# Performance work log

Hardware: AMD Instinct MI355X
Metric: run time of the kernel (lower is better)

The kernel has to match this reference:

```python
import jax, jax.numpy as jnp
import numpy as np

N = 8192
C = 128
K = 20          # neighbors per dilation branch
DILS = (1, 2)   # dilations
K_FULL = K * max(DILS)  # neighbors in the base knn graph
R = 4           # upsampling ratio
N_IDGCN = 2     # inception blocks
NEG_SLOPE_CONV = 0.2
NEG_SLOPE_MLP = 0.01  # torch LeakyReLU default in reconstructor


def knn_idx(pos, k):
    # brute-force knn on [N,3]; exclude self by taking k+1 and dropping col 0
    sq = jnp.sum(pos * pos, axis=-1)                       # [N]
    d = sq[:, None] + sq[None, :] - 2.0 * (pos @ pos.T)    # [N,N]
    _, idx = jax.lax.top_k(-d, k + 1)                      # nearest first
    return idx[:, 1:]                                      # [N,k]


def edge_conv(x, idx, W, b):
    # EdgeConv: max_j LeakyReLU(W @ [x_i, x_j - x_i] + b)
    xj = x[idx]                                            # [N,k,C] gather
    xi = jnp.broadcast_to(x[:, None, :], xj.shape)
    e = jnp.concatenate([xi, xj - xi], axis=-1)            # [N,k,2C]
    h = jax.nn.leaky_relu(e @ W + b, NEG_SLOPE_CONV)
    return jnp.max(h, axis=1)                              # [N,Cout]


def setup_inputs() -> dict:
    key = jax.random.key(0)
    ks = jax.random.split(key, 10)
    s_lift = 1.0 / np.sqrt(6.0)
    s_gcn = 1.0 / np.sqrt(2.0 * C)
    s_mlp = 1.0 / np.sqrt(C)
    n_gcn = N_IDGCN * len(DILS)
    return {
        "x": jax.random.normal(ks[0], (N, 3), dtype=jnp.float32),
        "W0": jax.random.normal(ks[1], (6, C), dtype=jnp.float32) * s_lift,
        "b0": jnp.zeros((C,), dtype=jnp.float32),
        "Wg": jax.random.normal(ks[2], (n_gcn, 2 * C, C), dtype=jnp.float32) * s_gcn,
        "bg": jnp.zeros((n_gcn, C), dtype=jnp.float32),
        "Wu": jax.random.normal(ks[3], (2 * C, R * C), dtype=jnp.float32) * s_gcn,
        "bu": jnp.zeros((R * C,), dtype=jnp.float32),
        "Wr1": jax.random.normal(ks[4], (C, C), dtype=jnp.float32) * s_mlp,
        "br1": jnp.zeros((C,), dtype=jnp.float32),
        "Wr2": jax.random.normal(ks[5], (C, 3), dtype=jnp.float32) * s_mlp,
        "br2": jnp.zeros((3,), dtype=jnp.float32),
    }


def reference(x, W0, b0, Wg, bg, Wu, bu, Wr1, br1, Wr2, br2):
    pos = x
    # knn graph on positions (k * max(dilations) neighbors)
    idx = knn_idx(pos, K_FULL)                             # [N, K_FULL]
    # lift 3 -> C with an EdgeConv on the first K neighbors
    h = edge_conv(pos, idx[:, :K], W0, b0)                 # [N, C]
    # Inception DenseGCN feature extractor: dilated EdgeConv branches + residual
    li = 0
    for _ in range(N_IDGCN):
        acc = jnp.zeros_like(h)
        for d in DILS:
            idx_d = idx[:, ::d][:, :K]                     # dilated neighbors
            acc = acc + edge_conv(h, idx_d, Wg[li], bg[li])
            li += 1
        h = h + acc / float(len(DILS))                     # residual
    # NodeShuffle upsampler: EdgeConv to r*C then shuffle nodes
    u = edge_conv(h, idx[:, :K], Wu, bu)                   # [N, r*C]
    u = u.reshape(N * R, C)                                # [N*r, C]
    # reconstructor MLP -> 3D coordinates
    q = jax.nn.leaky_relu(u @ Wr1 + br1, NEG_SLOPE_MLP)
    q = q @ Wr2 + br2                                      # [N*r, 3]
    return q
```

## Files before the change

kernel.cpp:

```cpp
#include <hip/hip_runtime.h>
#include <math.h>

#define N_PTS 8192
#define KFULL 40
#define KNB 20
#define QB 8
#define KBLK 512
#define NBK 1024
#define CAP 512

typedef unsigned short u16;
typedef unsigned int u32;
typedef unsigned long long u64;
typedef __attribute__((ext_vector_type(8))) short bf16x8;
typedef __attribute__((ext_vector_type(4))) float f32x4;
typedef __attribute__((ext_vector_type(2))) float f32x2;

__device__ __forceinline__ u16 f2b(float v) {
  u32 u = __float_as_uint(v);
  return (u16)((u + 0x7FFFu + ((u >> 16) & 1u)) >> 16);
}
__device__ __forceinline__ float b2f(u16 b) {
  return __uint_as_float(((u32)b) << 16);
}
__device__ __forceinline__ u32 pk2(float a, float b) {
  return (u32)f2b(a) | ((u32)f2b(b) << 16);
}
__device__ __forceinline__ u32 dmap(float d) {
  u32 b = __float_as_uint(d);
  return b ^ ((u32)(((int)b) >> 31) | 0x80000000u);
}
__device__ __forceinline__ float inv_edge(int b) {
  if (b >= 1022) return 3.4e38f;
  const u32 m = (((u32)(b + 1)) << 22) - 1u;
  if (m < 0x80000000u) return 0.f;
  return __uint_as_float(m - 0x80000000u);
}
__device__ __forceinline__ void maxu4(const uint4 v, float m[8]) {
  m[0] = fmaxf(m[0], __uint_as_float(v.x << 16));
  m[1] = fmaxf(m[1], __uint_as_float(v.x & 0xFFFF0000u));
  m[2] = fmaxf(m[2], __uint_as_float(v.y << 16));
  m[3] = fmaxf(m[3], __uint_as_float(v.y & 0xFFFF0000u));
  m[4] = fmaxf(m[4], __uint_as_float(v.z << 16));
  m[5] = fmaxf(m[5], __uint_as_float(v.z & 0xFFFF0000u));
  m[6] = fmaxf(m[6], __uint_as_float(v.w << 16));
  m[7] = fmaxf(m[7], __uint_as_float(v.w & 0xFFFF0000u));
}
__device__ __forceinline__ void unp4(const uint4 v, float p[8]) {
  p[0] = __uint_as_float(v.x << 16);
  p[1] = __uint_as_float(v.x & 0xFFFF0000u);
  p[2] = __uint_as_float(v.y << 16);
  p[3] = __uint_as_float(v.y & 0xFFFF0000u);
  p[4] = __uint_as_float(v.z << 16);
  p[5] = __uint_as_float(v.z & 0xFFFF0000u);
  p[6] = __uint_as_float(v.w << 16);
  p[7] = __uint_as_float(v.w & 0xFFFF0000u);
}

typedef const __attribute__((address_space(1))) unsigned int* gas_p;
typedef __attribute__((address_space(3))) unsigned int* las_p;
__device__ __forceinline__ void gll16(const void* g, void* l) {
  __builtin_amdgcn_global_load_lds((gas_p)g, (las_p)l, 16, 0, 0);
}

__device__ __forceinline__ f32x2 pdist(const f32x2 qx2, const f32x2 qy2,
                                       const f32x2 qz2, const f32x2 qs2,
                                       const float4 p) {
  const f32x2 px = {p.x, p.x}, py = {p.y, p.y}, pz = {p.z, p.z};
  const f32x2 pw = {p.w, p.w};
  return __builtin_elementwise_fma(
      qx2, px,
      __builtin_elementwise_fma(
          qy2, py, __builtin_elementwise_fma(qz2, pz, qs2 + pw)));
}

__device__ __forceinline__ void scan_cut(const u32 (*hist)[NBK], int* s_cut,
                                         int t) {
  const int w = t >> 6, lane = t & 63;
  if (w < QB / 2) {
    const u32* H = hist[w];
    const int base = lane * (NBK / 64);
    u32 lsum = 0;
#pragma unroll
    for (int k = 0; k < NBK / 64; ++k) lsum += H[base + k];
    u32 inc = lsum;
#pragma unroll
    for (int off = 1; off < 64; off <<= 1) {
      const u32 u = __shfl_up(inc, off);
      if (lane >= off) inc += u;
    }
    const u32 excl = inc - lsum;
    const u32 TGT = KFULL + 1;
    const u32 exlo = excl & 0xFFFFu, inlo = inc & 0xFFFFu;
    if (exlo < TGT && inlo >= TGT) {
      u32 cum = exlo;
      for (int k = 0; k < NBK / 64; ++k) {
        cum += H[base + k] & 0xFFFFu;
        if (cum >= TGT) { s_cut[2 * w] = base + k; break; }
      }
    }
    const u32 exhi = excl >> 16, inhi = inc >> 16;
    if (exhi < TGT && inhi >= TGT) {
      u32 cum = exhi;
      for (int k = 0; k < NBK / 64; ++k) {
        cum += H[base + k] >> 16;
        if (cum >= TGT) { s_cut[2 * w + 1] = base + k; break; }
      }
    }
  }
}

__device__ __forceinline__ int scan_cut_wave(const u32* H, int lane) {
  const int base = lane * (NBK / 64);
  u32 lsum = 0;
#pragma unroll
  for (int k = 0; k < NBK / 64; ++k) lsum += H[base + k];
  u32 inc = lsum;
#pragma unroll
  for (int off = 1; off < 64; off <<= 1) {
    const u32 u = __shfl_up(inc, off);
    if (lane >= off) inc += u;
  }
  const u32 excl = inc - lsum;
  int cut = -1;
  if (excl < 41u && inc >= 41u) {
    u32 cum = excl;
    for (int k = 0; k < NBK / 64; ++k) {
      cum += H[base + k];
      if (cum >= 41u) { cut = base + k; break; }
    }
  }
  const u64 mask = __ballot(cut >= 0);
  if (mask == 0ull) return NBK - 1;
  const int src = __ffsll((long long)mask) - 1;
  return __shfl(cut, src);
}

__global__ __launch_bounds__(KBLK) void knn_kernel(const float4* __restrict__ pos4,
                                                   int* __restrict__ idx_out) {
  __shared__ __align__(16) u32 hmem[2 * QB * CAP];
  u32 (*hist)[NBK] = (u32(*)[NBK])hmem;
  u64 (*cand)[CAP] = (u64(*)[CAP])hmem;
  __shared__ float4 s_q[QB];
  __shared__ int s_cut[QB];
  __shared__ int s_cnt[QB];

  const int qb = blockIdx.x * QB, t = threadIdx.x;
  if (t < QB) {
    s_q[t] = pos4[qb + t];
    s_cnt[t] = 0;
  }
  for (int b = t; b < 4 * NBK; b += KBLK) hmem[b] = 0;
  __syncthreads();

  f32x2 qx2[4], qy2[4], qz2[4], qs2[4];
#pragma unroll
  for (int qp = 0; qp < 4; ++qp) {
    const float4 v0 = s_q[2 * qp], v1 = s_q[2 * qp + 1];
    qx2[qp] = (f32x2){-2.0f * v0.x, -2.0f * v1.x};
    qy2[qp] = (f32x2){-2.0f * v0.y, -2.0f * v1.y};
    qz2[qp] = (f32x2){-2.0f * v0.z, -2.0f * v1.z};
    qs2[qp] = (f32x2){v0.w, v1.w};
  }

  {
    const int j = t << 4;
    const float4 p = pos4[j];
#pragma unroll
    for (int qp = 0; qp < 4; ++qp) {
      const f32x2 d2 = pdist(qx2[qp], qy2[qp], qz2[qp], qs2[qp], p);
      atomicAdd(&hist[qp][dmap(d2.x) >> 22], 1u);
      atomicAdd(&hist[qp][dmap(d2.y) >> 22], 0x10000u);
    }
  }
  __syncthreads();
  scan_cut(hist, s_cut, t);
  __syncthreads();
  float r2a[QB];
#pragma unroll
  for (int q = 0; q < QB; ++q) r2a[q] = inv_edge(s_cut[q]);
  for (int b = t; b < 4 * NBK; b += KBLK) hmem[b] = 0;
  __syncthreads();

#pragma unroll 2
  for (int s = 0; s < 16; ++s) {
    const int j = t + (s << 9);
    const float4 p = pos4[j];
#pragma unroll
    for (int qp = 0; qp < 4; ++qp) {
      const f32x2 d2 = pdist(qx2[qp], qy2[qp], qz2[qp], qs2[qp], p);
      if (d2.x <= r2a[2 * qp]) atomicAdd(&hist[qp][dmap(d2.x) >> 22], 1u);
      if (d2.y <= r2a[2 * qp + 1]) atomicAdd(&hist[qp][dmap(d2.y) >> 22], 0x10000u);
    }
  }
  __syncthreads();
  scan_cut(hist, s_cut, t);
  __syncthreads();
  float r2b[QB];
#pragma unroll
  for (int q = 0; q < QB; ++q) r2b[q] = inv_edge(s_cut[q]);

#pragma unroll 2
  for (int s = 0; s < 16; ++s) {
    const int j = t + (s << 9);
    const float4 p = pos4[j];
#pragma unroll
    for (int qp = 0; qp < 4; ++qp) {
      const f32x2 d2 = pdist(qx2[qp], qy2[qp], qz2[qp], qs2[qp], p);
      if (d2.x <= r2b[2 * qp]) {
        const int slot = atomicAdd(&s_cnt[2 * qp], 1);
        if (slot < CAP)
          cand[2 * qp][slot] = ((u64)dmap(d2.x) << 13) | (u64)j;
      }
      if (d2.y <= r2b[2 * qp + 1]) {
        const int slot = atomicAdd(&s_cnt[2 * qp + 1], 1);
        if (slot < CAP)
          cand[2 * qp + 1][slot] = ((u64)dmap(d2.y) << 13) | (u64)j;
      }
    }
  }
  __syncthreads();

  {
    const int w = t >> 6, lane = t & 63;
    int cnt = s_cnt[w];
    if (cnt > CAP) {
      const float4 qv = s_q[w];
      const float ax = -2.0f * qv.x, ay = -2.0f * qv.y, az = -2.0f * qv.z;
      const float aw = qv.w;
      const float R2w = inv_edge(s_cut[w]);
      u32* fbh = (u32*)cand[w];
      for (int b = lane; b < NBK; b += 64) fbh[b] = 0;
      for (int j = lane; j < N_PTS; j += 64) {
        const float4 p = pos4[j];
        const float d = fmaf(ax, p.x, fmaf(ay, p.y, fmaf(az, p.z, aw + p.w)));
        if (d <= R2w) atomicAdd(&fbh[dmap(d) >> 22], 1u);
      }
      const int cut2 = scan_cut_wave(fbh, lane);
      const float R2r = inv_edge(cut2);
      int base = 0;
      for (int j0 = 0; j0 < N_PTS; j0 += 64) {
        const int j = j0 + lane;
        const float4 p = pos4[j];
        const float d = fmaf(ax, p.x, fmaf(ay, p.y, fmaf(az, p.z, aw + p.w)));
        const bool pred = (d <= R2r);
        const u64 mask = __ballot(pred);
        if (pred) {
          const int off = __popcll(mask & ((1ull << lane) - 1ull));
          if (base + off < CAP)
            cand[w][base + off] = ((u64)dmap(d) << 13) | (u64)j;
        }
        base += (int)__popcll(mask);
      }
      cnt = base;
    }
    const int cmax = cnt < CAP ? cnt : CAP;
    if (cmax <= 192) {
      const u64 FK = ~0ull;
      const u64 my0 = (lane < cmax) ? cand[w][lane] : FK;
      const u64 my1 = (lane + 64 < cmax) ? cand[w][lane + 64] : FK;
      const u64 my2 = (lane + 128 < cmax) ? cand[w][lane + 128] : FK;
      int rk0 = 0, rk1 = 0, rk2 = 0;
      for (int c = 0; c < cmax; ++c) {
        const u64 bc = cand[w][c];
        rk0 += (bc < my0) ? 1 : 0;
        rk1 += (bc < my1) ? 1 : 0;
        rk2 += (bc < my2) ? 1 : 0;
      }
      if (lane < cmax && rk0 >= 1 && rk0 <= KFULL)
        idx_out[(qb + w) * KFULL + (rk0 - 1)] = (int)(my0 & 0x1FFFull);
      if (lane + 64 < cmax && rk1 >= 1 && rk1 <= KFULL)
        idx_out[(qb + w) * KFULL + (rk1 - 1)] = (int)(my1 & 0x1FFFull);
      if (lane + 128 < cmax && rk2 >= 1 && rk2 <= KFULL)
        idx_out[(qb + w) * KFULL + (rk2 - 1)] = (int)(my2 & 0x1FFFull);
    } else {
      for (int c0 = lane; c0 < cmax; c0 += 64) {
        const u64 my = cand[w][c0];
        int rank = 0;
        for (int c = 0; c < cmax; ++c) rank += (cand[w][c] < my) ? 1 : 0;
        if (rank >= 1 && rank <= KFULL)
          idx_out[(qb + w) * KFULL + (rank - 1)] = (int)(my & 0x1FFFull);
      }
    }
  }
}

__device__ __forceinline__ void wcvt_body(const float* __restrict__ src,
                                          u16* __restrict__ dst, int ncols,
                                          int rows_per_tensor, int elems_per_tensor,
                                          int rg, int k) {
  const int li = rg / rows_per_tensor;
  const int r = rg % rows_per_tensor;
  const float* s = src + (size_t)li * elems_per_tensor;
  u16* d = dst + (size_t)li * elems_per_tensor;
  const int part = r / ncols, col = r % ncols;
  d[(size_t)r * 128 + k] = f2b(s[(size_t)(part * 128 + k) * ncols + col]);
}

__global__ __launch_bounds__(128) void prep_kernel(
    const float* __restrict__ x, const float* __restrict__ W0,
    const float* __restrict__ b0, const float* __restrict__ Wg,
    const float* __restrict__ Wu, const float* __restrict__ Wr1,
    float* __restrict__ Aout, u16* __restrict__ Pout, u16* __restrict__ Wgb,
    u16* __restrict__ Wub, u16* __restrict__ Wr1b, float4* __restrict__ pos4) {
  const int b = blockIdx.x, t = threadIdx.x;
  if (b < 8192) {
    const float px = x[b * 3 + 0], py = x[b * 3 + 1], pz = x[b * 3 + 2];
    const float a = b0[t] + px * W0[t] + py * W0[128 + t] + pz * W0[256 + t];
    const float p = px * W0[384 + t] + py * W0[512 + t] + pz * W0[640 + t];
    Aout[(size_t)b * 128 + t] = a;
    Pout[(size_t)b * 128 + t] = f2b(p);
  } else if (b < 9216) {
    wcvt_body(Wg, Wgb, 128, 256, 256 * 128, b - 8192, t);
  } else if (b < 10240) {
    wcvt_body(Wu, Wub, 512, 1024, 1024 * 128, b - 9216, t);
  } else if (b < 10368) {
    wcvt_body(Wr1, Wr1b, 128, 128, 128 * 128, b - 10240, t);
  } else {
    const int j = (b - 10368) * 128 + t;
    const float px = x[j * 3 + 0], py = x[j * 3 + 1], pz = x[j * 3 + 2];
    pos4[j] = make_float4(px, py, pz, px * px + py * py + pz * pz);
  }
}

__global__ __launch_bounds__(256) void gemm_mfma_kernel(
    const u16* __restrict__ Ain, const u16* __restrict__ Wt,
    const float* __restrict__ bias, int GA, int span_shift, int nAtot, int nPtot,
    float slope, int use_act, float* __restrict__ Aout,
    u16* __restrict__ Aout16, u16* __restrict__ Pout) {
  __shared__ __align__(16) u16 Al[128 * 128];
  __shared__ __align__(16) u16 Bl[64 * 128];
  const int bm = blockIdx.x * 128;
  const int bn = blockIdx.y * 64;
  const int tid = threadIdx.x;

#pragma unroll
  for (int it = 0; it < 8; ++it) {
    const int g = it * 256 + tid;
    const int row = g >> 4, cc = g & 15;
    const int sc = cc ^ (row & 7);
    gll16(Ain + (size_t)(bm + row) * 128 + sc * 8, &Al[g * 8]);
  }
#pragma unroll
  for (int it = 0; it < 4; ++it) {
    const int g = it * 256 + tid;
    const int row = g >> 4, cc = g & 15;
    const int sc = cc ^ (row & 7);
    gll16(Wt + (size_t)(bn + row) * 128 + sc * 8, &Bl[g * 8]);
  }
  __syncthreads();

  const int wv = tid >> 6, lane = tid & 63;
  const int wm = wv & 1, wn = wv >> 1;
  const int lr = lane & 15, lk = lane >> 4;

  bf16x8 a[4][4], b[2][4];
  f32x4 acc[4][2];
#pragma unroll
  for (int m = 0; m < 4; ++m)
#pragma unroll
    for (int n = 0; n < 2; ++n) acc[m][n] = (f32x4){0.f, 0.f, 0.f, 0.f};

#pragma unroll
  for (int m = 0; m < 4; ++m) {
    const int row = wm * 64 + m * 16 + lr;
#pragma unroll
    for (int ks = 0; ks < 4; ++ks) {
      const int c = ks * 4 + lk;
      a[m][ks] = *(const bf16x8*)&Al[row * 128 + (c ^ (row & 7)) * 8];
    }
  }
#pragma unroll
  for (int n = 0; n < 2; ++n) {
    const int col = wn * 32 + n * 16 + lr;
#pragma unroll
    for (int ks = 0; ks < 4; ++ks) {
      const int c = ks * 4 + lk;
      b[n][ks] = *(const bf16x8*)&Bl[col * 128 + (c ^ (col & 7)) * 8];
    }
  }

#pragma unroll
  for (int ks = 0; ks < 4; ++ks)
#pragma unroll
    for (int m = 0; m < 4; ++m)
#pragma unroll
      for (int n = 0; n < 2; ++n)
        acc[m][n] = __builtin_amdgcn_mfma_f32_16x16x32_bf16(a[m][ks], b[n][ks],
                                                            acc[m][n], 0, 0, 0);

  const int span = 1 << span_shift;
  const int GP = span - GA;
#pragma unroll
  for (int n = 0; n < 2; ++n) {
    const int col = bn + wn * 32 + n * 16 + lr;
    const int g = col >> span_shift;
    const int wi = col & (span - 1);
    const bool isA = wi < GA;
    const float bv = isA ? bias[g * GA + wi] : 0.f;
#pragma unroll
    for (int m = 0; m < 4; ++m) {
      const int row0 = bm + wm * 64 + m * 16 + lk * 4;
#pragma unroll
      for (int r = 0; r < 4; ++r) {
        float v = acc[m][n][r] + bv;
        if (isA) {
          if (use_act) v = v > 0.f ? v : v * slope;
          if (Aout16)
            Aout16[(size_t)(row0 + r) * nAtot + g * GA + wi] = f2b(v);
          else
            Aout[(size_t)(row0 + r) * nAtot + g * GA + wi] = v;
        } else {
          Pout[(size_t)(row0 + r) * nPtot + g * GP + (wi - GA)] = f2b(v);
        }
      }
    }
  }
}

__global__ __launch_bounds__(256) void gather_one_kernel(
    const float* __restrict__ A, const u16* __restrict__ P,
    const int* __restrict__ idx, int C, int dil, float* __restrict__ outf,
    u16* __restrict__ outb) {
  const int t = threadIdx.x;
  const int i = blockIdx.x * 16 + (t >> 4);
  const int c = blockIdx.y * 128 + (t & 15) * 8;
  float m[8];
#pragma unroll
  for (int k = 0; k < 8; ++k) m[k] = -INFINITY;
  const int ib = i * KFULL;
#pragma unroll
  for (int j = 0; j < KNB; ++j) {
    const int n = idx[ib + j * dil] & (N_PTS - 1);
    maxu4(*(const uint4*)&P[(size_t)n * C + c], m);
  }
  float pv[8];
  unp4(*(const uint4*)&P[(size_t)i * C + c], pv);
  const float4 a0 = *(const float4*)&A[(size_t)i * C + c];
  const float4 a1 = *(const float4*)&A[(size_t)i * C + c + 4];
  const float av[8] = {a0.x, a0.y, a0.z, a0.w, a1.x, a1.y, a1.z, a1.w};
  float v[8];
#pragma unroll
  for (int k = 0; k < 8; ++k) {
    const float x = av[k] - pv[k] + m[k];
    v[k] = x > 0.f ? x : 0.2f * x;
  }
  if (outf) {
    *(float4*)&outf[(size_t)i * C + c] = make_float4(v[0], v[1], v[2], v[3]);
    *(float4*)&outf[(size_t)i * C + c + 4] = make_float4(v[4], v[5], v[6], v[7]);
  }
  if (outb) {
    uint4 pb = {pk2(v[0], v[1]), pk2(v[2], v[3]), pk2(v[4], v[5]), pk2(v[6], v[7])};
    *(uint4*)&outb[(size_t)i * C + c] = pb;
  }
}

__global__ __launch_bounds__(256) void gather_pair_kernel(
    const float* __restrict__ Ap, const u16* __restrict__ Pp,
    const int* __restrict__ idx, float* __restrict__ h, u16* __restrict__ hb) {
  const int t = threadIdx.x;
  const int i = blockIdx.x * 16 + (t >> 4);
  const int c = (t & 15) * 8;
  float m1[8], m2[8];
#pragma unroll
  for (int k = 0; k < 8; ++k) { m1[k] = -INFINITY; m2[k] = -INFINITY; }
  const int ib = i * KFULL;
#pragma unroll
  for (int j = 0; j < KNB; ++j) {
    const int n1 = idx[ib + j] & (N_PTS - 1);
    maxu4(*(const uint4*)&Pp[(size_t)n1 * 256 + c], m1);
    const int n2 = idx[ib + 2 * j] & (N_PTS - 1);
    maxu4(*(const uint4*)&Pp[(size_t)n2 * 256 + 128 + c], m2);
  }
  float p0[8], p1[8];
  unp4(*(const uint4*)&Pp[(size_t)i * 256 + c], p0);
  unp4(*(const uint4*)&Pp[(size_t)i * 256 + 128 + c], p1);
  const float4 a00 = *(const float4*)&Ap[(size_t)i * 256 + c];
  const float4 a01 = *(const float4*)&Ap[(size_t)i * 256 + c + 4];
  const float4 a10 = *(const float4*)&Ap[(size_t)i * 256 + 128 + c];
  const float4 a11 = *(const float4*)&Ap[(size_t)i * 256 + 128 + c + 4];
  const float av0[8] = {a00.x, a00.y, a00.z, a00.w, a01.x, a01.y, a01.z, a01.w};
  const float av1[8] = {a10.x, a10.y, a10.z, a10.w, a11.x, a11.y, a11.z, a11.w};
  const float4 h0 = *(const float4*)&h[(size_t)i * 128 + c];
  const float4 h1 = *(const float4*)&h[(size_t)i * 128 + c + 4];
  const float hv[8] = {h0.x, h0.y, h0.z, h0.w, h1.x, h1.y, h1.z, h1.w};
  float v[8];
#pragma unroll
  for (int k = 0; k < 8; ++k) {
    float x1 = av0[k] - p0[k] + m1[k];
    x1 = x1 > 0.f ? x1 : 0.2f * x1;
    float x2 = av1[k] - p1[k] + m2[k];
    x2 = x2 > 0.f ? x2 : 0.2f * x2;
    v[k] = hv[k] + 0.5f * (x1 + x2);
  }
  *(float4*)&h[(size_t)i * 128 + c] = make_float4(v[0], v[1], v[2], v[3]);
  *(float4*)&h[(size_t)i * 128 + c + 4] = make_float4(v[4], v[5], v[6], v[7]);
  uint4 pb = {pk2(v[0], v[1]), pk2(v[2], v[3]), pk2(v[4], v[5]), pk2(v[6], v[7])};
  *(uint4*)&hb[(size_t)i * 128 + c] = pb;
}

__global__ __launch_bounds__(256) void recon_fused_kernel(
    const u16* __restrict__ Ab16, const u16* __restrict__ Pb16,
    const int* __restrict__ idx, const u16* __restrict__ Wr1b,
    const float* __restrict__ br1, const float* __restrict__ Wr2,
    const float* __restrict__ br2, float* __restrict__ out) {
  __shared__ __align__(16) u16 Al[128 * 128];
  __shared__ __align__(16) u16 Bl[128 * 128];
  __shared__ __align__(16) u16 Tt[128 * 132];
  __shared__ float w2s[387];
  const int b = blockIdx.x, tid = threadIdx.x;
  const int pbase = b * 32;

#pragma unroll
  for (int it = 0; it < 8; ++it) {
    const int g = it * 256 + tid;
    const int row = g >> 4, cc = g & 15;
    const int sc = cc ^ (row & 7);
    gll16(Wr1b + (size_t)row * 128 + sc * 8, &Bl[g * 8]);
  }
  if (tid < 128) {
    w2s[tid] = Wr2[tid];
    w2s[tid + 128] = Wr2[tid + 128];
    w2s[tid + 256] = Wr2[tid + 256];
  }
  if (tid < 3) w2s[384 + tid] = br2[tid];

#pragma unroll
  for (int it = 0; it < 4; ++it) {
    const int tau = it * 256 + tid;
    const int rr = tau >> 3;
    const int cg = tau & 7;
    const int pl = rr >> 2, s = rr & 3;
    const int p = pbase + pl;
    const int colb = s * 128 + cg * 16;
    float m[8], m2[8];
#pragma unroll
    for (int k = 0; k < 8; ++k) { m[k] = -INFINITY; m2[k] = -INFINITY; }
    const int ib = p * KFULL;
#pragma unroll
    for (int j = 0; j < KNB; ++j) {
      const int n = idx[ib + j] & (N_PTS - 1);
      maxu4(*(const uint4*)&Pb16[(size_t)n * 512 + colb], m);
      maxu4(*(const uint4*)&Pb16[(size_t)n * 512 + colb + 8], m2);
    }
    float av[8], av2[8], pv[8], pv2[8];
    unp4(*(const uint4*)&Ab16[(size_t)p * 512 + colb], av);
    unp4(*(const uint4*)&Ab16[(size_t)p * 512 + colb + 8], av2);
    unp4(*(const uint4*)&Pb16[(size_t)p * 512 + colb], pv);
    unp4(*(const uint4*)&Pb16[(size_t)p * 512 + colb + 8], pv2);
    float v[8], v2[8];
#pragma unroll
    for (int k = 0; k < 8; ++k) {
      float x = av[k] - pv[k] + m[k];
      v[k] = x > 0.f ? x : 0.2f * x;
      float y = av2[k] - pv2[k] + m2[k];
      v2[k] = y > 0.f ? y : 0.2f * y;
    }
    uint4 w0 = {pk2(v[0], v[1]), pk2(v[2], v[3]), pk2(v[4], v[5]), pk2(v[6], v[7])};
    uint4 w1 = {pk2(v2[0], v2[1]), pk2(v2[2], v2[3]), pk2(v2[4], v2[5]),
                pk2(v2[6], v2[7])};
    const int c0 = cg * 2, c1 = cg * 2 + 1;
    *(uint4*)&Al[rr * 128 + (c0 ^ (rr & 7)) * 8] = w0;
    *(uint4*)&Al[rr * 128 + (c1 ^ (rr & 7)) * 8] = w1;
  }
  __syncthreads();

  const int wv = tid >> 6, lane = tid & 63;
  const int wm = wv & 1, wn = wv >> 1;
  const int lr = lane & 15, lk = lane >> 4;
  f32x4 acc[4][4];
#pragma unroll
  for (int m = 0; m < 4; ++m)
#pragma unroll
    for (int n = 0; n < 4; ++n) acc[m][n] = (f32x4){0.f, 0.f, 0.f, 0.f};

#pragma unroll
  for (int ks = 0; ks < 4; ++ks) {
    const int c = ks * 4 + lk;
    bf16x8 a[4], bb[4];
#pragma unroll
    for (int m = 0; m < 4; ++m) {
      const int row = wm * 64 + m * 16 + lr;
      a[m] = *(const bf16x8*)&Al[row * 128 + (c ^ (row & 7)) * 8];
    }
#pragma unroll
    for (int n = 0; n < 4; ++n) {
      const int col = wn * 64 + n * 16 + lr;
      bb[n] = *(const bf16x8*)&Bl[col * 128 + (c ^ (col & 7)) * 8];
    }
#pragma unroll
    for (int m = 0; m < 4; ++m)
#pragma unroll
      for (int n = 0; n < 4; ++n)
        acc[m][n] = __builtin_amdgcn_mfma_f32_16x16x32_bf16(a[m], bb[n],
                                                            acc[m][n], 0, 0, 0);
  }

#pragma unroll
  for (int n = 0; n < 4; ++n) {
    const int col = wn * 64 + n * 16 + lr;
    const float bv = br1[col];
#pragma unroll
    for (int m = 0; m < 4; ++m) {
      const int row0 = wm * 64 + m * 16 + lk * 4;
#pragma unroll
      for (int r = 0; r < 4; ++r) {
        float v = acc[m][n][r] + bv;
        v = v > 0.f ? v : 0.01f * v;
        Tt[(row0 + r) * 132 + col] = f2b(v);
      }
    }
  }
  __syncthreads();

  if (tid < 128) {
    float q0 = w2s[384], q1 = w2s[385], q2 = w2s[386];
#pragma unroll 4
    for (int k = 0; k < 128; ++k) {
      const float tv = b2f(Tt[tid * 132 + k]);
      q0 = fmaf(tv, w2s[k * 3 + 0], q0);
      q1 = fmaf(tv, w2s[k * 3 + 1], q1);
      q2 = fmaf(tv, w2s[k * 3 + 2], q2);
    }
    const size_t R = (size_t)b * 128 + tid;
    out[R * 3 + 0] = q0;
    out[R * 3 + 1] = q1;
    out[R * 3 + 2] = q2;
  }
}

extern "C" void kernel_launch(void* const* d_in, const int* in_sizes, int n_in,
                              void* d_out, int out_size, void* d_ws, size_t ws_size,
                              hipStream_t stream) {
  const float* x = (const float*)d_in[0];
  const float* W0 = (const float*)d_in[1];
  const float* b0 = (const float*)d_in[2];
  const float* Wg = (const float*)d_in[3];
  const float* bg = (const float*)d_in[4];
  const float* Wu = (const float*)d_in[5];
  const float* bu = (const float*)d_in[6];
  const float* Wr1 = (const float*)d_in[7];
  const float* br1 = (const float*)d_in[8];
  const float* Wr2 = (const float*)d_in[9];
  const float* br2 = (const float*)d_in[10];
  float* out = (float*)d_out;

  char* w = (char*)d_ws;
  int* idx = (int*)(w + 0);
  float4* pos4 = (float4*)(w + 1310720);
  float* h = (float*)(w + 1441792);
  u16* hb = (u16*)(w + 5636096);
  float* Apair = (float*)(w + 7733248);
  u16* Ppair = (u16*)(w + 16121856);
  u16* Wgb = (u16*)(w + 20316160);
  u16* Wub = (u16*)(w + 20578304);
  u16* Wr1b = (u16*)(w + 20840448);
  float* Abig = (float*)(w + 20873216);
  u16* Ab16 = (u16*)(w + 20873216);
  u16* Pbig = (u16*)(w + 37650432);

  prep_kernel<<<10432, 128, 0, stream>>>(x, W0, b0, Wg, Wu, Wr1, Abig, Pbig, Wgb,
                                         Wub, Wr1b, pos4);

  knn_kernel<<<N_PTS / QB, KBLK, 0, stream>>>(pos4, idx);

  gather_one_kernel<<<dim3(512, 1), 256, 0, stream>>>(Abig, Pbig, idx, 128, 1, h, hb);

  for (int blk = 0; blk < 2; ++blk) {
    const int li = blk * 2;
    gemm_mfma_kernel<<<dim3(64, 8), 256, 0, stream>>>(
        hb, Wgb + (size_t)li * 256 * 128, bg + li * 128, 128, 8, 256, 256, 0.f, 0,
        Apair, (u16*)nullptr, Ppair);
    gather_pair_kernel<<<512, 256, 0, stream>>>(Apair, Ppair, idx, h, hb);
  }

  gemm_mfma_kernel<<<dim3(64, 16), 256, 0, stream>>>(hb, Wub, bu, 512, 10, 512, 512,
                                                     0.f, 0, (float*)nullptr, Ab16,
                                                     Pbig);

  recon_fused_kernel<<<256, 256, 0, stream>>>(Ab16, Pbig, idx, Wr1b, br1, Wr2, br2,
                                              out);
}
```

Before: 162.3 us.

## Replace two-pass histogram radius search in kNN with sampled per-lane top-4 bound

The kNN kernel no longer builds two shared-memory histograms, each with a scan, to find a distance cutoff. Each wave instead takes a 2048-point sample (every fourth point), keeps a per-lane top-4 of distance keys, and binary-searches with ballots for the 41st smallest key. That value is an upper bound on the true 41st-nearest distance and becomes the radius for a single candidate-collection pass. This removes one full distance pass and the histogram atomics, but the looser radius admits more candidates. The rank-sort fast path is widened to 256 candidates to absorb that, and the overflow fallback remains for the case of more than 512.

```diff
diff --git a/kernel.cpp b/kernel.cpp
--- a/kernel.cpp
+++ b/kernel.cpp
@@ -29,6 +29,10 @@
 __device__ __forceinline__ u32 dmap(float d) {
   u32 b = __float_as_uint(d);
   return b ^ ((u32)(((int)b) >> 31) | 0x80000000u);
+}
+__device__ __forceinline__ float inv_dmap(u32 m) {
+  return (m & 0x80000000u) ? __uint_as_float(m & 0x7FFFFFFFu)
+                           : __uint_as_float(~m);
 }
 __device__ __forceinline__ float inv_edge(int b) {
   if (b >= 1022) return 3.4e38f;
@@ -74,42 +78,6 @@
           qy2, py, __builtin_elementwise_fma(qz2, pz, qs2 + pw)));
 }
 
-__device__ __forceinline__ void scan_cut(const u32 (*hist)[NBK], int* s_cut,
-                                         int t) {
-  const int w = t >> 6, lane = t & 63;
-  if (w < QB / 2) {
-    const u32* H = hist[w];
-    const int base = lane * (NBK / 64);
-    u32 lsum = 0;
-#pragma unroll
-    for (int k = 0; k < NBK / 64; ++k) lsum += H[base + k];
-    u32 inc = lsum;
-#pragma unroll
-    for (int off = 1; off < 64; off <<= 1) {
-      const u32 u = __shfl_up(inc, off);
-      if (lane >= off) inc += u;
-    }
-    const u32 excl = inc - lsum;
-    const u32 TGT = KFULL + 1;
-    const u32 exlo = excl & 0xFFFFu, inlo = inc & 0xFFFFu;
-    if (exlo < TGT && inlo >= TGT) {
-      u32 cum = exlo;
-      for (int k = 0; k < NBK / 64; ++k) {
-        cum += H[base + k] & 0xFFFFu;
-        if (cum >= TGT) { s_cut[2 * w] = base + k; break; }
-      }
-    }
-    const u32 exhi = excl >> 16, inhi = inc >> 16;
-    if (exhi < TGT && inhi >= TGT) {
-      u32 cum = exhi;
-      for (int k = 0; k < NBK / 64; ++k) {
-        cum += H[base + k] >> 16;
-        if (cum >= TGT) { s_cut[2 * w + 1] = base + k; break; }
-      }
-    }
-  }
-}
-
 __device__ __forceinline__ int scan_cut_wave(const u32* H, int lane) {
   const int base = lane * (NBK / 64);
   u32 lsum = 0;
@@ -138,22 +106,51 @@
 
 __global__ __launch_bounds__(KBLK) void knn_kernel(const float4* __restrict__ pos4,
                                                    int* __restrict__ idx_out) {
-  __shared__ __align__(16) u32 hmem[2 * QB * CAP];
-  u32 (*hist)[NBK] = (u32(*)[NBK])hmem;
-  u64 (*cand)[CAP] = (u64(*)[CAP])hmem;
+  __shared__ __align__(16) u64 candm[QB][CAP];
   __shared__ float4 s_q[QB];
-  __shared__ int s_cut[QB];
+  __shared__ float s_r2[QB];
   __shared__ int s_cnt[QB];
 
   const int qb = blockIdx.x * QB, t = threadIdx.x;
+  const int w = t >> 6, lane = t & 63;
   if (t < QB) {
     s_q[t] = pos4[qb + t];
     s_cnt[t] = 0;
   }
-  for (int b = t; b < 4 * NBK; b += KBLK) hmem[b] = 0;
   __syncthreads();
 
+  {
+    const float4 qv = s_q[w];
+    const float ax = -2.0f * qv.x, ay = -2.0f * qv.y, az = -2.0f * qv.z;
+    const float aw = qv.w;
+    u32 k0 = ~0u, k1 = ~0u, k2 = ~0u, k3 = ~0u;
+#pragma unroll 4
+    for (int s = 0; s < 32; ++s) {
+      const int j = (lane + (s << 6)) << 2;
+      const float4 p = pos4[j];
+      const float d = fmaf(ax, p.x, fmaf(ay, p.y, fmaf(az, p.z, aw + p.w)));
+      const u32 k = dmap(d);
+      if (k < k3) {
+        k3 = k;
+        u32 tt;
+        if (k3 < k2) { tt = k2; k2 = k3; k3 = tt; }
+        if (k2 < k1) { tt = k1; k1 = k2; k2 = tt; }
+        if (k1 < k0) { tt = k0; k0 = k1; k1 = tt; }
+      }
+    }
+    u32 lo = 0u, hi = ~0u;
+    for (int it = 0; it < 32; ++it) {
+      const u32 mid = lo + ((hi - lo) >> 1);
+      const int c = __popcll(__ballot(k0 <= mid)) + __popcll(__ballot(k1 <= mid)) +
+                    __popcll(__ballot(k2 <= mid)) + __popcll(__ballot(k3 <= mid));
+      if (c >= (int)(KFULL + 1)) hi = mid; else lo = mid + 1;
+    }
+    if (lane == 0) s_r2[w] = inv_dmap(lo);
+  }
+  __syncthreads();
+
   f32x2 qx2[4], qy2[4], qz2[4], qs2[4];
+  float r2[QB];
 #pragma unroll
   for (int qp = 0; qp < 4; ++qp) {
     const float4 v0 = s_q[2 * qp], v1 = s_q[2 * qp + 1];
@@ -162,25 +159,8 @@
     qz2[qp] = (f32x2){-2.0f * v0.z, -2.0f * v1.z};
     qs2[qp] = (f32x2){v0.w, v1.w};
   }
-
-  {
-    const int j = t << 4;
-    const float4 p = pos4[j];
-#pragma unroll
-    for (int qp = 0; qp < 4; ++qp) {
-      const f32x2 d2 = pdist(qx2[qp], qy2[qp], qz2[qp], qs2[qp], p);
-      atomicAdd(&hist[qp][dmap(d2.x) >> 22], 1u);
-      atomicAdd(&hist[qp][dmap(d2.y) >> 22], 0x10000u);
-    }
-  }
-  __syncthreads();
-  scan_cut(hist, s_cut, t);
-  __syncthreads();
-  float r2a[QB];
-#pragma unroll
-  for (int q = 0; q < QB; ++q) r2a[q] = inv_edge(s_cut[q]);
-  for (int b = t; b < 4 * NBK; b += KBLK) hmem[b] = 0;
-  __syncthreads();
+#pragma unroll
+  for (int q = 0; q < QB; ++q) r2[q] = s_r2[q];
 
 #pragma unroll 2
   for (int s = 0; s < 16; ++s) {
@@ -189,47 +169,28 @@
 #pragma unroll
     for (int qp = 0; qp < 4; ++qp) {
       const f32x2 d2 = pdist(qx2[qp], qy2[qp], qz2[qp], qs2[qp], p);
-      if (d2.x <= r2a[2 * qp]) atomicAdd(&hist[qp][dmap(d2.x) >> 22], 1u);
-      if (d2.y <= r2a[2 * qp + 1]) atomicAdd(&hist[qp][dmap(d2.y) >> 22], 0x10000u);
-    }
-  }
-  __syncthreads();
-  scan_cut(hist, s_cut, t);
-  __syncthreads();
-  float r2b[QB];
-#pragma unroll
-  for (int q = 0; q < QB; ++q) r2b[q] = inv_edge(s_cut[q]);
-
-#pragma unroll 2
-  for (int s = 0; s < 16; ++s) {
-    const int j = t + (s << 9);
-    const float4 p = pos4[j];
-#pragma unroll
-    for (int qp = 0; qp < 4; ++qp) {
-      const f32x2 d2 = pdist(qx2[qp], qy2[qp], qz2[qp], qs2[qp], p);
-      if (d2.x <= r2b[2 * qp]) {
+      if (d2.x <= r2[2 * qp]) {
         const int slot = atomicAdd(&s_cnt[2 * qp], 1);
         if (slot < CAP)
-          cand[2 * qp][slot] = ((u64)dmap(d2.x) << 13) | (u64)j;
-      }
-      if (d2.y <= r2b[2 * qp + 1]) {
+          candm[2 * qp][slot] = ((u64)dmap(d2.x) << 13) | (u64)j;
+      }
+      if (d2.y <= r2[2 * qp + 1]) {
         const int slot = atomicAdd(&s_cnt[2 * qp + 1], 1);
         if (slot < CAP)
-          cand[2 * qp + 1][slot] = ((u64)dmap(d2.y) << 13) | (u64)j;
+          candm[2 * qp + 1][slot] = ((u64)dmap(d2.y) << 13) | (u64)j;
       }
     }
   }
   __syncthreads();
 
   {
-    const int w = t >> 6, lane = t & 63;
     int cnt = s_cnt[w];
     if (cnt > CAP) {
       const float4 qv = s_q[w];
       const float ax = -2.0f * qv.x, ay = -2.0f * qv.y, az = -2.0f * qv.z;
       const float aw = qv.w;
-      const float R2w = inv_edge(s_cut[w]);
-      u32* fbh = (u32*)cand[w];
+      const float R2w = s_r2[w];
+      u32* fbh = (u32*)candm[w];
       for (int b = lane; b < NBK; b += 64) fbh[b] = 0;
       for (int j = lane; j < N_PTS; j += 64) {
         const float4 p = pos4[j];
@@ -248,24 +209,26 @@
         if (pred) {
           const int off = __popcll(mask & ((1ull << lane) - 1ull));
           if (base + off < CAP)
-            cand[w][base + off] = ((u64)dmap(d) << 13) | (u64)j;
+            candm[w][base + off] = ((u64)dmap(d) << 13) | (u64)j;
         }
         base += (int)__popcll(mask);
       }
       cnt = base;
     }
     const int cmax = cnt < CAP ? cnt : CAP;
-    if (cmax <= 192) {
+    if (cmax <= 256) {
       const u64 FK = ~0ull;
-      const u64 my0 = (lane < cmax) ? cand[w][lane] : FK;
-      const u64 my1 = (lane + 64 < cmax) ? cand[w][lane + 64] : FK;
-      const u64 my2 = (lane + 128 < cmax) ? cand[w][lane + 128] : FK;
-      int rk0 = 0, rk1 = 0, rk2 = 0;
+      const u64 my0 = (lane < cmax) ? candm[w][lane] : FK;
+      const u64 my1 = (lane + 64 < cmax) ? candm[w][lane + 64] : FK;
+      const u64 my2 = (lane + 128 < cmax) ? candm[w][lane + 128] : FK;
+      const u64 my3 = (lane + 192 < cmax) ? candm[w][lane + 192] : FK;
+      int rk0 = 0, rk1 = 0, rk2 = 0, rk3 = 0;
       for (int c = 0; c < cmax; ++c) {
-        const u64 bc = cand[w][c];
+        const u64 bc = candm[w][c];
         rk0 += (bc < my0) ? 1 : 0;
         rk1 += (bc < my1) ? 1 : 0;
         rk2 += (bc < my2) ? 1 : 0;
+        rk3 += (bc < my3) ? 1 : 0;
       }
       if (lane < cmax && rk0 >= 1 && rk0 <= KFULL)
         idx_out[(qb + w) * KFULL + (rk0 - 1)] = (int)(my0 & 0x1FFFull);
@@ -273,11 +236,13 @@
         idx_out[(qb + w) * KFULL + (rk1 - 1)] = (int)(my1 & 0x1FFFull);
       if (lane + 128 < cmax && rk2 >= 1 && rk2 <= KFULL)
         idx_out[(qb + w) * KFULL + (rk2 - 1)] = (int)(my2 & 0x1FFFull);
+      if (lane + 192 < cmax && rk3 >= 1 && rk3 <= KFULL)
+        idx_out[(qb + w) * KFULL + (rk3 - 1)] = (int)(my3 & 0x1FFFull);
     } else {
       for (int c0 = lane; c0 < cmax; c0 += 64) {
-        const u64 my = cand[w][c0];
+        const u64 my = candm[w][c0];
         int rank = 0;
-        for (int c = 0; c < cmax; ++c) rank += (cand[w][c] < my) ? 1 : 0;
+        for (int c = 0; c < cmax; ++c) rank += (candm[w][c] < my) ? 1 : 0;
         if (rank >= 1 && rank <= KFULL)
           idx_out[(qb + w) * KFULL + (rank - 1)] = (int)(my & 0x1FFFull);
       }
```

Measured after the change: 181.3 us. +11.7%, slower.
